# Performance work log

Measured on AMD Instinct MI355X. Metric: run time of the kernel, lower is better.

## Reference

```python
import jax, jax.numpy as jnp
import numpy as np
import math

B, S, D, H = 4, 2048, 1024, 16
DK = D // H
DFF = 1024  # FeedForward default d_ff=1024 (DecoderLayer passes only d_model)
EPS = 1e-6
SQRT_2_OVER_PI = math.sqrt(2.0 / math.pi)


def setup_inputs() -> dict:
    key = jax.random.key(0)
    ks = jax.random.split(key, 12)
    sc = 0.02
    x = jax.random.normal(ks[0], (B, S, D), dtype=jnp.float32)
    # causal look-ahead mask: 1 where attendable, 0 where masked
    mask = jnp.broadcast_to(jnp.tril(jnp.ones((S, S), dtype=jnp.int32)), (B, S, S))
    inp = {
        'x': x,
        'mask': mask,
        'Wq': jax.random.normal(ks[1], (D, D), jnp.float32) * sc,
        'bq': jnp.zeros((D,), jnp.float32),
        'Wk': jax.random.normal(ks[2], (D, D), jnp.float32) * sc,
        'bk': jnp.zeros((D,), jnp.float32),
        'Wv': jax.random.normal(ks[3], (D, D), jnp.float32) * sc,
        'bv': jnp.zeros((D,), jnp.float32),
        'Wo': jax.random.normal(ks[4], (D, D), jnp.float32) * sc,
        'bo': jnp.zeros((D,), jnp.float32),
        'W1': jax.random.normal(ks[5], (D, DFF), jnp.float32) * sc,
        'b1': jnp.zeros((DFF,), jnp.float32),
        'W2': jax.random.normal(ks[6], (DFF, D), jnp.float32) * sc,
        'b2': jnp.zeros((D,), jnp.float32),
        'alpha1': jnp.ones((D,), jnp.float32),
        'bias1': jnp.zeros((D,), jnp.float32),
        'alpha2': jnp.ones((D,), jnp.float32),
        'bias2': jnp.zeros((D,), jnp.float32),
    }
    return inp


def _norm(x, alpha, bias):
    # torch: (x - mean) / (x.std(unbiased=True) + eps) * alpha + bias
    mean = jnp.mean(x, axis=-1, keepdims=True)
    var = jnp.sum((x - mean) ** 2, axis=-1, keepdims=True) / (x.shape[-1] - 1)
    std = jnp.sqrt(var)
    return alpha * (x - mean) / (std + EPS) + bias


def _gelu(x):
    return 0.5 * x * (1.0 + jnp.tanh(SQRT_2_OVER_PI * (x + 0.044715 * x ** 3)))


def reference(x, mask, Wq, bq, Wk, bk, Wv, bv, Wo, bo, W1, b1, W2, b2,
              alpha1, bias1, alpha2, bias2):
    b, s, d = x.shape
    x2 = _norm(x, alpha1, bias1)
    q = (x2 @ Wq + bq).reshape(b, s, H, DK).transpose(0, 2, 1, 3)  # bhsd
    k = (x2 @ Wk + bk).reshape(b, s, H, DK).transpose(0, 2, 1, 3)
    v = (x2 @ Wv + bv).reshape(b, s, H, DK).transpose(0, 2, 1, 3)
    scores = jnp.einsum('bhqd,bhkd->bhqk', q, k) / jnp.sqrt(jnp.float32(DK))
    scores = jnp.where(mask[:, None, :, :] == 0, jnp.float32(-1e9), scores)
    probs = jax.nn.softmax(scores, axis=-1)
    attn = jnp.einsum('bhqk,bhkd->bhqd', probs, v)
    concat = attn.transpose(0, 2, 1, 3).reshape(b, s, d)
    x = x + (concat @ Wo + bo)
    x2 = _norm(x, alpha2, bias2)
    ff = _gelu(x2 @ W1 + b1) @ W2 + b2
    return x + ff
```

## Files before the change

### kernel.cpp

```cpp
#include <hip/hip_runtime.h>
#include <hip/hip_bf16.h>
#include <math.h>


#define B_ 4
#define S_ 2048
#define D_ 1024
#define H_ 16
#define DFF_ 1024

typedef __attribute__((ext_vector_type(8))) short short8;
typedef __attribute__((ext_vector_type(8))) unsigned short ushort8;
typedef __attribute__((ext_vector_type(4))) float f32x4;

__device__ __forceinline__ unsigned short f2bf(float f) {
  __hip_bfloat16 h = __float2bfloat16(f);
  return *reinterpret_cast<unsigned short*>(&h);
}

__device__ __forceinline__ void gload16(const void* g, void* l) {
  __builtin_amdgcn_global_load_lds(
      (const __attribute__((address_space(1))) void*)g,
      (__attribute__((address_space(3))) void*)l, 16, 0, 0);
}

__global__ __launch_bounds__(256) void tcast6_k(
    const float* s0, const float* s1, const float* s2, const float* s3,
    const float* s4, const float* s5, unsigned short* d0, unsigned short* d1,
    unsigned short* d2, unsigned short* d3, unsigned short* d4,
    unsigned short* d5) {
  const float* src;
  unsigned short* dst;
  switch (blockIdx.z) {
    case 0: src = s0; dst = d0; break;
    case 1: src = s1; dst = d1; break;
    case 2: src = s2; dst = d2; break;
    case 3: src = s3; dst = d3; break;
    case 4: src = s4; dst = d4; break;
    default: src = s5; dst = d5; break;
  }
  __shared__ float tile[64][65];
  const int k0 = blockIdx.y * 64, n0 = blockIdx.x * 64;
  const int t = threadIdx.x;
  const int r = t >> 2, c0 = (t & 3) * 16;
  const float4* sp =
      reinterpret_cast<const float4*>(src + (size_t)(k0 + r) * 1024 + n0 + c0);
#pragma unroll
  for (int j = 0; j < 4; ++j) {
    float4 v = sp[j];
    tile[r][c0 + 4 * j] = v.x;
    tile[r][c0 + 4 * j + 1] = v.y;
    tile[r][c0 + 4 * j + 2] = v.z;
    tile[r][c0 + 4 * j + 3] = v.w;
  }
  __syncthreads();
  ushort8 o0, o1;
#pragma unroll
  for (int j = 0; j < 8; ++j) o0[j] = f2bf(tile[c0 + j][r]);
#pragma unroll
  for (int j = 0; j < 8; ++j) o1[j] = f2bf(tile[c0 + 8 + j][r]);
  unsigned short* dp = dst + (size_t)(n0 + r) * 1024 + k0 + c0;
  *reinterpret_cast<ushort8*>(dp) = o0;
  *reinterpret_cast<ushort8*>(dp + 8) = o1;
}

__global__ __launch_bounds__(256) void ln_k(const float* __restrict__ x,
                                            const float* __restrict__ alpha,
                                            const float* __restrict__ bias,
                                            unsigned short* __restrict__ out) {
  int row = blockIdx.x, t = threadIdx.x;
  float4 v = reinterpret_cast<const float4*>(x + (size_t)row * D_)[t];
  float s = v.x + v.y + v.z + v.w;
  float q = v.x * v.x + v.y * v.y + v.z * v.z + v.w * v.w;
#pragma unroll
  for (int off = 32; off > 0; off >>= 1) {
    s += __shfl_down(s, off);
    q += __shfl_down(q, off);
  }
  __shared__ float ss[4], sq[4], stat[2];
  if ((t & 63) == 0) { ss[t >> 6] = s; sq[t >> 6] = q; }
  __syncthreads();
  if (t == 0) {
    float S = ss[0] + ss[1] + ss[2] + ss[3];
    float Q = sq[0] + sq[1] + sq[2] + sq[3];
    float mean = S * (1.0f / D_);
    float var = fmaxf((Q - D_ * mean * mean) * (1.0f / (D_ - 1)), 0.0f);
    stat[0] = mean;
    stat[1] = 1.0f / (sqrtf(var) + 1e-6f);
  }
  __syncthreads();
  float mean = stat[0], inv = stat[1];
  float4 a = reinterpret_cast<const float4*>(alpha)[t];
  float4 b = reinterpret_cast<const float4*>(bias)[t];
  ushort4 o;
  o.x = f2bf((v.x - mean) * inv * a.x + b.x);
  o.y = f2bf((v.y - mean) * inv * a.y + b.y);
  o.z = f2bf((v.z - mean) * inv * a.z + b.z);
  o.w = f2bf((v.w - mean) * inv * a.w + b.w);
  reinterpret_cast<ushort4*>(out + (size_t)row * D_)[t] = o;
}

__device__ __forceinline__ void gemm_core64(
    const unsigned short* __restrict__ A, const unsigned short* __restrict__ Wt,
    int m0, int n0, int K, unsigned short* As ,
    unsigned short* Bs , f32x4 (&acc)[2][4]) {
  const int t = threadIdx.x;
  const int wv = t >> 6, lane = t & 63, quad = lane >> 4, l16 = lane & 15;
  const int wm = wv >> 1, wn = wv & 1;
  const int lr8 = lane >> 3;
  const int lseg = ((lane & 7) ^ lr8) * 8;

  const unsigned short* Ag0 = A + (size_t)(m0 + wv * 16 + lr8) * K + lseg;
  const unsigned short* Ag1 = A + (size_t)(m0 + wv * 16 + 8 + lr8) * K + lseg;
  const unsigned short* Bg0 = Wt + (size_t)(n0 + wv * 32 + lr8) * K + lseg;
  const unsigned short* Bg1 = Wt + (size_t)(n0 + wv * 32 + 8 + lr8) * K + lseg;
  const unsigned short* Bg2 = Wt + (size_t)(n0 + wv * 32 + 16 + lr8) * K + lseg;
  const unsigned short* Bg3 = Wt + (size_t)(n0 + wv * 32 + 24 + lr8) * K + lseg;
  unsigned short* Al0 = &As[(wv * 16) * 64];
  unsigned short* Al1 = &As[(wv * 16 + 8) * 64];
  unsigned short* Bl0 = &Bs[(wv * 32) * 64];
  unsigned short* Bl1 = &Bs[(wv * 32 + 8) * 64];
  unsigned short* Bl2 = &Bs[(wv * 32 + 16) * 64];
  unsigned short* Bl3 = &Bs[(wv * 32 + 24) * 64];

  for (int k0 = 0; k0 < K; k0 += 64) {
    gload16(Ag0, Al0);
    gload16(Ag1, Al1);
    gload16(Bg0, Bl0);
    gload16(Bg1, Bl1);
    gload16(Bg2, Bl2);
    gload16(Bg3, Bl3);
    __syncthreads();
    short8 af[2][2], bf[2][4];
#pragma unroll
    for (int p = 0; p < 2; ++p) {
#pragma unroll
      for (int mt = 0; mt < 2; ++mt) {
        int r = wm * 32 + mt * 16 + l16;
        af[p][mt] = *reinterpret_cast<const short8*>(
            &As[r * 64 + (((p * 4 + quad) ^ (r & 7)) << 3)]);
      }
#pragma unroll
      for (int nt = 0; nt < 4; ++nt) {
        int r = wn * 64 + nt * 16 + l16;
        bf[p][nt] = *reinterpret_cast<const short8*>(
            &Bs[r * 64 + (((p * 4 + quad) ^ (r & 7)) << 3)]);
      }
    }
#pragma unroll
    for (int p = 0; p < 2; ++p)
#pragma unroll
      for (int mt = 0; mt < 2; ++mt)
#pragma unroll
        for (int nt = 0; nt < 4; ++nt)
          acc[mt][nt] = __builtin_amdgcn_mfma_f32_16x16x32_bf16(
              af[p][mt], bf[p][nt], acc[mt][nt], 0, 0, 0);
    __syncthreads();
    Ag0 += 64; Ag1 += 64; Bg0 += 64; Bg1 += 64; Bg2 += 64; Bg3 += 64;
  }
}

__global__ __launch_bounds__(256, 4) void gemm_k(
    const unsigned short* __restrict__ A, const unsigned short* __restrict__ Wt,
    const float* __restrict__ bias, const float* __restrict__ res,
    void* __restrict__ outp, int M, int N, int K, int flags) {
  __shared__ unsigned short As[64 * 64];
  __shared__ unsigned short Bs[128 * 64];
  const int t = threadIdx.x;
  const int m0 = blockIdx.y * 64, n0 = blockIdx.x * 128;
  const int wv = t >> 6, lane = t & 63, quad = lane >> 4, l16 = lane & 15;
  const int wm = wv >> 1, wn = wv & 1;
  f32x4 acc[2][4] = {};
  gemm_core64(A, Wt, m0, n0, K, As, Bs, acc);

  const bool obf = flags & 1, dog = flags & 2;
#pragma unroll
  for (int nt = 0; nt < 4; ++nt) {
    int col = n0 + wn * 64 + nt * 16 + l16;
    float bv = bias[col];
#pragma unroll
    for (int mt = 0; mt < 2; ++mt) {
#pragma unroll
      for (int r = 0; r < 4; ++r) {
        int row = m0 + wm * 32 + mt * 16 + quad * 4 + r;
        float v = acc[mt][nt][r] + bv;
        if (res) v += res[(size_t)row * N + col];
        if (dog) {
          float e = __expf(1.5957691216057308f * (v + 0.044715f * v * v * v));
          float th = 1.0f - 2.0f / (1.0f + e);
          v = 0.5f * v * (1.0f + th);
        }
        if (obf)
          ((unsigned short*)outp)[(size_t)row * N + col] = f2bf(v);
        else
          ((float*)outp)[(size_t)row * N + col] = v;
      }
    }
  }
}

__global__ __launch_bounds__(256, 4) void gemmqkv_k(
    const unsigned short* __restrict__ A, const unsigned short* __restrict__ Wt,
    const float* __restrict__ bq, const float* __restrict__ bk,
    const float* __restrict__ bv, unsigned short* __restrict__ outq,
    unsigned short* __restrict__ outk, unsigned short* __restrict__ outvt,
    int M, int K) {
  __shared__ unsigned short As[64 * 64];
  __shared__ unsigned short Bs[128 * 64];
  const int t = threadIdx.x;
  const int m0 = blockIdx.y * 64, n0 = blockIdx.x * 128;
  const int wv = t >> 6, lane = t & 63, quad = lane >> 4, l16 = lane & 15;
  const int wm = wv >> 1, wn = wv & 1;
  f32x4 acc[2][4] = {};
  gemm_core64(A, Wt, m0, n0, K, As, Bs, acc);

  const int seg = n0 >> 10;
  const int nb = n0 & 1023;
  const float* bias = (seg == 0) ? bq : (seg == 1) ? bk : bv;
  if (seg < 2) {
    unsigned short* o = (seg == 0) ? outq : outk;
#pragma unroll
    for (int nt = 0; nt < 4; ++nt) {
      int col = nb + wn * 64 + nt * 16 + l16;
      float bvv = bias[col];
#pragma unroll
      for (int mt = 0; mt < 2; ++mt)
#pragma unroll
        for (int r = 0; r < 4; ++r) {
          int row = m0 + wm * 32 + mt * 16 + quad * 4 + r;
          o[(size_t)row * D_ + col] = f2bf(acc[mt][nt][r] + bvv);
        }
    }
  } else {
#pragma unroll
    for (int nt = 0; nt < 4; ++nt) {
      int col = nb + wn * 64 + nt * 16 + l16;
      float bvv = bias[col];
      int h = col >> 6, dk = col & 63;
#pragma unroll
      for (int mt = 0; mt < 2; ++mt) {
        int m = m0 + wm * 32 + mt * 16 + quad * 4;
        int b = m >> 11, sidx = m & 2047;
        ushort4 o;
        o.x = f2bf(acc[mt][nt][0] + bvv);
        o.y = f2bf(acc[mt][nt][1] + bvv);
        o.z = f2bf(acc[mt][nt][2] + bvv);
        o.w = f2bf(acc[mt][nt][3] + bvv);
        *reinterpret_cast<ushort4*>(
            &outvt[(((size_t)(b * 16 + h) * 64 + dk) * 2048 + sidx)]) = o;
      }
    }
  }
}

__global__ __launch_bounds__(256, 2) void attn_k(
    const unsigned short* __restrict__ Q, const unsigned short* __restrict__ Kg,
    const unsigned short* __restrict__ VT, unsigned short* __restrict__ Og) {
  __shared__ unsigned short Ks[2][64 * 64];
  __shared__ unsigned short Vs[2][64 * 64];
  __shared__ unsigned short Ps[4 * 32 * 72];
  const int t = threadIdx.x;
  const int pair = blockIdx.x >> 6, bh = blockIdx.x & 63;
  const int b = bh >> 4, h = bh & 15;
  const int hi = 31 - pair, lo = pair;
  const int w = t >> 6, lane = t & 63, quad = lane >> 4, l16 = lane & 15;
  const int qhi0 = hi * 64 + w * 16, qlo0 = lo * 64 + w * 16;
  unsigned short* PsW = &Ps[w * 32 * 72];

  short8 qfh[2], qfl[2];
#pragma unroll
  for (int kc = 0; kc < 2; ++kc) {
    qfh[kc] = *reinterpret_cast<const short8*>(
        Q + (size_t)(b * S_ + qhi0 + l16) * D_ + h * 64 + kc * 32 + quad * 8);
    qfl[kc] = *reinterpret_cast<const short8*>(
        Q + (size_t)(b * S_ + qlo0 + l16) * D_ + h * 64 + kc * 32 + quad * 8);
  }
  asm volatile("" ::"v"(qfh[0]), "v"(qfh[1]), "v"(qfl[0]), "v"(qfl[1])
               : "memory");

  f32x4 Oh[4] = {}, Ol[4] = {};
  float lh_acc = 0.0f, ll_acc = 0.0f;

  const int srA = w * 8 + (lane >> 3);
  const int ssA = ((lane & 7) ^ (srA & 7)) * 8;
  const int srB = srA + 32;
  const int ssB = ((lane & 7) ^ (srB & 7)) * 8;
  const unsigned short* KgA = Kg + (size_t)(b * S_ + srA) * D_ + h * 64 + ssA;
  const unsigned short* KgB = Kg + (size_t)(b * S_ + srB) * D_ + h * 64 + ssB;
  const unsigned short* VgA = VT + ((size_t)bh * 64 + srA) * 2048 + ssA;
  const unsigned short* VgB = VT + ((size_t)bh * 64 + srB) * 2048 + ssB;
  unsigned short* KlA = &Ks[0][(w * 8) * 64];
  unsigned short* KlB = &Ks[0][(32 + w * 8) * 64];
  unsigned short* VlA = &Vs[0][(w * 8) * 64];
  unsigned short* VlB = &Vs[0][(32 + w * 8) * 64];

  const float C0 = 0.18033688011f;
  const float C1 = -23.08312065f;

  gload16(KgA, KlA);
  gload16(KgB, KlB);
  gload16(VgA, VlA);
  gload16(VgB, VlB);
  KgA += (size_t)64 * D_;
  KgB += (size_t)64 * D_;
  VgA += 64;
  VgB += 64;

  for (int kt = 0; kt <= hi; ++kt) {
    const int k0 = kt * 64;
    const bool dolo = (kt <= lo);
    const int coff = (kt & 1) << 12;
    const int noff = ((kt & 1) ^ 1) << 12;

    if (kt < hi) {
      gload16(KgA, KlA + noff);
      gload16(KgB, KlB + noff);
      gload16(VgA, VlA + noff);
      gload16(VgB, VlB + noff);
      KgA += (size_t)64 * D_;
      KgB += (size_t)64 * D_;
      VgA += 64;
      VgB += 64;
      asm volatile("s_waitcnt vmcnt(4)" ::: "memory");
    } else {
      asm volatile("s_waitcnt vmcnt(0)" ::: "memory");
    }
    asm volatile("s_barrier" ::: "memory");

    const unsigned short* Ksc = &Ks[0][coff];
    const unsigned short* Vsc = &Vs[0][coff];

    f32x4 sch[4] = {}, scl[4] = {};
#pragma unroll
    for (int mt = 0; mt < 4; ++mt) {
      int r = mt * 16 + l16;
      short8 kf0 = *reinterpret_cast<const short8*>(
          &Ksc[r * 64 + ((quad ^ (r & 7)) << 3)]);
      short8 kf1 = *reinterpret_cast<const short8*>(
          &Ksc[r * 64 + (((4 + quad) ^ (r & 7)) << 3)]);
      sch[mt] = __builtin_amdgcn_mfma_f32_16x16x32_bf16(kf0, qfh[0], sch[mt],
                                                        0, 0, 0);
      sch[mt] = __builtin_amdgcn_mfma_f32_16x16x32_bf16(kf1, qfh[1], sch[mt],
                                                        0, 0, 0);
      if (dolo) {
        scl[mt] = __builtin_amdgcn_mfma_f32_16x16x32_bf16(kf0, qfl[0], scl[mt],
                                                          0, 0, 0);
        scl[mt] = __builtin_amdgcn_mfma_f32_16x16x32_bf16(kf1, qfl[1], scl[mt],
                                                          0, 0, 0);
      }
    }

    {
      const bool diag = (kt == hi);
      const int q = qhi0 + l16;
#pragma unroll
      for (int mt = 0; mt < 4; ++mt) {
        float pv[4];
#pragma unroll
        for (int r = 0; r < 4; ++r) {
          int key = k0 + mt * 16 + quad * 4 + r;
          float p = __builtin_amdgcn_exp2f(fmaf(sch[mt][r], C0, C1));
          if (diag && key > q) p = 0.0f;
          lh_acc += p;
          pv[r] = p;
        }
        ushort4 pk = {f2bf(pv[0]), f2bf(pv[1]), f2bf(pv[2]), f2bf(pv[3])};
        *reinterpret_cast<ushort4*>(&PsW[l16 * 72 + mt * 16 + quad * 4]) = pk;
      }
    }
    if (dolo) {
      const bool diag = (kt == lo);
      const int q = qlo0 + l16;
#pragma unroll
      for (int mt = 0; mt < 4; ++mt) {
        float pv[4];
#pragma unroll
        for (int r = 0; r < 4; ++r) {
          int key = k0 + mt * 16 + quad * 4 + r;
          float p = __builtin_amdgcn_exp2f(fmaf(scl[mt][r], C0, C1));
          if (diag && key > q) p = 0.0f;
          ll_acc += p;
          pv[r] = p;
        }
        ushort4 pk = {f2bf(pv[0]), f2bf(pv[1]), f2bf(pv[2]), f2bf(pv[3])};
        *reinterpret_cast<ushort4*>(
            &PsW[(16 + l16) * 72 + mt * 16 + quad * 4]) = pk;
      }
    }
    __builtin_amdgcn_sched_barrier(0);

    short8 pfh[2], pfl[2];
#pragma unroll
    for (int kc = 0; kc < 2; ++kc)
      pfh[kc] = *reinterpret_cast<const short8*>(
          &PsW[l16 * 72 + kc * 32 + quad * 8]);
    if (dolo) {
#pragma unroll
      for (int kc = 0; kc < 2; ++kc)
        pfl[kc] = *reinterpret_cast<const short8*>(
            &PsW[(16 + l16) * 72 + kc * 32 + quad * 8]);
    }

#pragma unroll
    for (int kc = 0; kc < 2; ++kc) {
#pragma unroll
      for (int nd = 0; nd < 4; ++nd) {
        int r = nd * 16 + l16;
        short8 vf = *reinterpret_cast<const short8*>(
            &Vsc[r * 64 + (((kc * 4 + quad) ^ (r & 7)) << 3)]);
        Oh[nd] = __builtin_amdgcn_mfma_f32_16x16x32_bf16(pfh[kc], vf, Oh[nd],
                                                         0, 0, 0);
        if (dolo)
          Ol[nd] = __builtin_amdgcn_mfma_f32_16x16x32_bf16(pfl[kc], vf, Ol[nd],
                                                           0, 0, 0);
      }
    }
    asm volatile("s_barrier" ::: "memory");
  }

  lh_acc += __shfl_xor(lh_acc, 16);
  lh_acc += __shfl_xor(lh_acc, 32);
  ll_acc += __shfl_xor(ll_acc, 16);
  ll_acc += __shfl_xor(ll_acc, 32);

#pragma unroll
  for (int r = 0; r < 4; ++r) {
    float lh = __shfl(lh_acc, quad * 4 + r);
    float ll = __shfl(ll_acc, quad * 4 + r);
    float rlh = 1.0f / lh, rll = 1.0f / ll;
#pragma unroll
    for (int nd = 0; nd < 4; ++nd) {
      Og[(size_t)(b * S_ + qhi0 + quad * 4 + r) * D_ + h * 64 + nd * 16 + l16] =
          f2bf(Oh[nd][r] * rlh);
      Og[(size_t)(b * S_ + qlo0 + quad * 4 + r) * D_ + h * 64 + nd * 16 + l16] =
          f2bf(Ol[nd][r] * rll);
    }
  }
}

extern "C" void kernel_launch(void* const* d_in, const int* in_sizes, int n_in,
                              void* d_out, int out_size, void* d_ws,
                              size_t ws_size, hipStream_t stream) {
  const float* x = (const float*)d_in[0];
  const float* Wq = (const float*)d_in[2];
  const float* bq = (const float*)d_in[3];
  const float* Wk = (const float*)d_in[4];
  const float* bk = (const float*)d_in[5];
  const float* Wv = (const float*)d_in[6];
  const float* bv = (const float*)d_in[7];
  const float* Wo = (const float*)d_in[8];
  const float* bo = (const float*)d_in[9];
  const float* W1 = (const float*)d_in[10];
  const float* b1 = (const float*)d_in[11];
  const float* W2 = (const float*)d_in[12];
  const float* b2 = (const float*)d_in[13];
  const float* alpha1 = (const float*)d_in[14];
  const float* bias1 = (const float*)d_in[15];
  const float* alpha2 = (const float*)d_in[16];
  const float* bias2 = (const float*)d_in[17];
  float* out = (float*)d_out;

  char* ws = (char*)d_ws;
  const size_t MB = 1024 * 1024;
  unsigned short* wqT = (unsigned short*)(ws + 0 * MB);
  unsigned short* wkT = (unsigned short*)(ws + 2 * MB);
  unsigned short* wvT = (unsigned short*)(ws + 4 * MB);
  unsigned short* woT = (unsigned short*)(ws + 6 * MB);
  unsigned short* w1T = (unsigned short*)(ws + 8 * MB);
  unsigned short* w2T = (unsigned short*)(ws + 10 * MB);
  unsigned short* x2a = (unsigned short*)(ws + 12 * MB);
  unsigned short* qb = (unsigned short*)(ws + 28 * MB);
  unsigned short* kb = (unsigned short*)(ws + 44 * MB);
  unsigned short* vtb = (unsigned short*)(ws + 60 * MB);

  tcast6_k<<<dim3(16, 16, 6), dim3(256), 0, stream>>>(Wq, Wk, Wv, Wo, W1, W2,
                                                      wqT, wkT, wvT, woT, w1T,
                                                      w2T);

  const int M = B_ * S_;
  ln_k<<<dim3(M), dim3(256), 0, stream>>>(x, alpha1, bias1, x2a);

  gemmqkv_k<<<dim3(24, 128), dim3(256), 0, stream>>>(x2a, wqT, bq, bk, bv, qb,
                                                     kb, vtb, M, D_);

  attn_k<<<dim3(1024), dim3(256), 0, stream>>>(qb, kb, vtb, x2a);

  dim3 gg(D_ / 128, M / 64);
  gemm_k<<<gg, dim3(256), 0, stream>>>(x2a, woT, bo, x, out, M, D_, D_, 0);

  ln_k<<<dim3(M), dim3(256), 0, stream>>>(out, alpha2, bias2, qb);

  gemm_k<<<gg, dim3(256), 0, stream>>>(qb, w1T, b1, nullptr, kb, M, DFF_, D_, 3);

  gemm_k<<<gg, dim3(256), 0, stream>>>(kb, w2T, b2, out, out, M, D_, DFF_, 0);
}
```

Measured before the change: 429.8 us.

## Split paired hi/lo attention blocks into one query tile per block; MFMA row sums

The attention kernel no longer pairs a high and a low query tile in one block. It launches 2048 blocks, each handling a single 64-query tile, ordered longest-first. The softmax denominator is now computed with an extra MFMA against a vector of ones, replacing the scalar accumulation and cross-lane shuffles. This raises parallelism and cuts register and LDS use, but each K/V tile loaded from memory now serves fewer queries and the causal work per block is uneven. The denominator also now sums bf16-rounded probabilities.

```diff
diff --git a/kernel.cpp b/kernel.cpp
--- a/kernel.cpp
+++ b/kernel.cpp
@@ -258,28 +258,27 @@
     const unsigned short* __restrict__ VT, unsigned short* __restrict__ Og) {
   __shared__ unsigned short Ks[2][64 * 64];
   __shared__ unsigned short Vs[2][64 * 64];
-  __shared__ unsigned short Ps[4 * 32 * 72];
+  __shared__ unsigned short Ps[4 * 16 * 72];
   const int t = threadIdx.x;
-  const int pair = blockIdx.x >> 6, bh = blockIdx.x & 63;
+  const int qt = 31 - (blockIdx.x >> 6);
+  const int bh = blockIdx.x & 63;
   const int b = bh >> 4, h = bh & 15;
-  const int hi = 31 - pair, lo = pair;
   const int w = t >> 6, lane = t & 63, quad = lane >> 4, l16 = lane & 15;
-  const int qhi0 = hi * 64 + w * 16, qlo0 = lo * 64 + w * 16;
-  unsigned short* PsW = &Ps[w * 32 * 72];
-
-  short8 qfh[2], qfl[2];
-#pragma unroll
-  for (int kc = 0; kc < 2; ++kc) {
-    qfh[kc] = *reinterpret_cast<const short8*>(
-        Q + (size_t)(b * S_ + qhi0 + l16) * D_ + h * 64 + kc * 32 + quad * 8);
-    qfl[kc] = *reinterpret_cast<const short8*>(
-        Q + (size_t)(b * S_ + qlo0 + l16) * D_ + h * 64 + kc * 32 + quad * 8);
-  }
-  asm volatile("" ::"v"(qfh[0]), "v"(qfh[1]), "v"(qfl[0]), "v"(qfl[1])
-               : "memory");
-
-  f32x4 Oh[4] = {}, Ol[4] = {};
-  float lh_acc = 0.0f, ll_acc = 0.0f;
+  const int q0 = qt * 64 + w * 16;
+  unsigned short* PsW = &Ps[w * 16 * 72];
+
+  short8 qf[2];
+#pragma unroll
+  for (int kc = 0; kc < 2; ++kc)
+    qf[kc] = *reinterpret_cast<const short8*>(
+        Q + (size_t)(b * S_ + q0 + l16) * D_ + h * 64 + kc * 32 + quad * 8);
+  asm volatile("" ::"v"(qf[0]), "v"(qf[1]) : "memory");
+
+  f32x4 Oh[4] = {};
+  f32x4 sums = {};
+  short8 onev;
+#pragma unroll
+  for (int j = 0; j < 8; ++j) onev[j] = (short)0x3F80;
 
   const int srA = w * 8 + (lane >> 3);
   const int ssA = ((lane & 7) ^ (srA & 7)) * 8;
@@ -306,13 +305,12 @@
   VgA += 64;
   VgB += 64;
 
-  for (int kt = 0; kt <= hi; ++kt) {
-    const int k0 = kt * 64;
-    const bool dolo = (kt <= lo);
+  for (int kt = 0; kt <= qt; ++kt) {
+    const bool diag = (kt == qt);
     const int coff = (kt & 1) << 12;
     const int noff = ((kt & 1) ^ 1) << 12;
 
-    if (kt < hi) {
+    if (kt < qt) {
       gload16(KgA, KlA + noff);
       gload16(KgB, KlB + noff);
       gload16(VgA, VlA + noff);
@@ -330,7 +328,7 @@
     const unsigned short* Ksc = &Ks[0][coff];
     const unsigned short* Vsc = &Vs[0][coff];
 
-    f32x4 sch[4] = {}, scl[4] = {};
+    f32x4 sch[4] = {};
 #pragma unroll
     for (int mt = 0; mt < 4; ++mt) {
       int r = mt * 16 + l16;
@@ -338,103 +336,60 @@
           &Ksc[r * 64 + ((quad ^ (r & 7)) << 3)]);
       short8 kf1 = *reinterpret_cast<const short8*>(
           &Ksc[r * 64 + (((4 + quad) ^ (r & 7)) << 3)]);
-      sch[mt] = __builtin_amdgcn_mfma_f32_16x16x32_bf16(kf0, qfh[0], sch[mt],
+      sch[mt] = __builtin_amdgcn_mfma_f32_16x16x32_bf16(kf0, qf[0], sch[mt],
                                                         0, 0, 0);
-      sch[mt] = __builtin_amdgcn_mfma_f32_16x16x32_bf16(kf1, qfh[1], sch[mt],
+      sch[mt] = __builtin_amdgcn_mfma_f32_16x16x32_bf16(kf1, qf[1], sch[mt],
                                                         0, 0, 0);
-      if (dolo) {
-        scl[mt] = __builtin_amdgcn_mfma_f32_16x16x32_bf16(kf0, qfl[0], scl[mt],
-                                                          0, 0, 0);
-        scl[mt] = __builtin_amdgcn_mfma_f32_16x16x32_bf16(kf1, qfl[1], scl[mt],
-                                                          0, 0, 0);
-      }
     }
 
     {
-      const bool diag = (kt == hi);
-      const int q = qhi0 + l16;
+      const int kb0 = kt * 64;
+      const int q = q0 + l16;
 #pragma unroll
       for (int mt = 0; mt < 4; ++mt) {
         float pv[4];
 #pragma unroll
         for (int r = 0; r < 4; ++r) {
-          int key = k0 + mt * 16 + quad * 4 + r;
+          int key = kb0 + mt * 16 + quad * 4 + r;
           float p = __builtin_amdgcn_exp2f(fmaf(sch[mt][r], C0, C1));
           if (diag && key > q) p = 0.0f;
-          lh_acc += p;
           pv[r] = p;
         }
         ushort4 pk = {f2bf(pv[0]), f2bf(pv[1]), f2bf(pv[2]), f2bf(pv[3])};
         *reinterpret_cast<ushort4*>(&PsW[l16 * 72 + mt * 16 + quad * 4]) = pk;
       }
     }
-    if (dolo) {
-      const bool diag = (kt == lo);
-      const int q = qlo0 + l16;
-#pragma unroll
-      for (int mt = 0; mt < 4; ++mt) {
-        float pv[4];
-#pragma unroll
-        for (int r = 0; r < 4; ++r) {
-          int key = k0 + mt * 16 + quad * 4 + r;
-          float p = __builtin_amdgcn_exp2f(fmaf(scl[mt][r], C0, C1));
-          if (diag && key > q) p = 0.0f;
-          ll_acc += p;
-          pv[r] = p;
-        }
-        ushort4 pk = {f2bf(pv[0]), f2bf(pv[1]), f2bf(pv[2]), f2bf(pv[3])};
-        *reinterpret_cast<ushort4*>(
-            &PsW[(16 + l16) * 72 + mt * 16 + quad * 4]) = pk;
-      }
-    }
     __builtin_amdgcn_sched_barrier(0);
 
-    short8 pfh[2], pfl[2];
+    short8 pf[2];
 #pragma unroll
     for (int kc = 0; kc < 2; ++kc)
-      pfh[kc] = *reinterpret_cast<const short8*>(
+      pf[kc] = *reinterpret_cast<const short8*>(
           &PsW[l16 * 72 + kc * 32 + quad * 8]);
-    if (dolo) {
-#pragma unroll
-      for (int kc = 0; kc < 2; ++kc)
-        pfl[kc] = *reinterpret_cast<const short8*>(
-            &PsW[(16 + l16) * 72 + kc * 32 + quad * 8]);
-    }
 
 #pragma unroll
     for (int kc = 0; kc < 2; ++kc) {
+      sums = __builtin_amdgcn_mfma_f32_16x16x32_bf16(pf[kc], onev, sums,
+                                                     0, 0, 0);
 #pragma unroll
       for (int nd = 0; nd < 4; ++nd) {
         int r = nd * 16 + l16;
         short8 vf = *reinterpret_cast<const short8*>(
             &Vsc[r * 64 + (((kc * 4 + quad) ^ (r & 7)) << 3)]);
-        Oh[nd] = __builtin_amdgcn_mfma_f32_16x16x32_bf16(pfh[kc], vf, Oh[nd],
+        Oh[nd] = __builtin_amdgcn_mfma_f32_16x16x32_bf16(pf[kc], vf, Oh[nd],
                                                          0, 0, 0);
-        if (dolo)
-          Ol[nd] = __builtin_amdgcn_mfma_f32_16x16x32_bf16(pfl[kc], vf, Ol[nd],
-                                                           0, 0, 0);
       }
     }
     asm volatile("s_barrier" ::: "memory");
   }
 
-  lh_acc += __shfl_xor(lh_acc, 16);
-  lh_acc += __shfl_xor(lh_acc, 32);
-  ll_acc += __shfl_xor(ll_acc, 16);
-  ll_acc += __shfl_xor(ll_acc, 32);
-
 #pragma unroll
   for (int r = 0; r < 4; ++r) {
-    float lh = __shfl(lh_acc, quad * 4 + r);
-    float ll = __shfl(ll_acc, quad * 4 + r);
-    float rlh = 1.0f / lh, rll = 1.0f / ll;
-#pragma unroll
-    for (int nd = 0; nd < 4; ++nd) {
-      Og[(size_t)(b * S_ + qhi0 + quad * 4 + r) * D_ + h * 64 + nd * 16 + l16] =
-          f2bf(Oh[nd][r] * rlh);
-      Og[(size_t)(b * S_ + qlo0 + quad * 4 + r) * D_ + h * 64 + nd * 16 + l16] =
-          f2bf(Ol[nd][r] * rll);
-    }
+    float rl = 1.0f / sums[r];
+#pragma unroll
+    for (int nd = 0; nd < 4; ++nd)
+      Og[(size_t)(b * S_ + q0 + quad * 4 + r) * D_ + h * 64 + nd * 16 + l16] =
+          f2bf(Oh[nd][r] * rl);
   }
 }
 
@@ -483,7 +438,7 @@
   gemmqkv_k<<<dim3(24, 128), dim3(256), 0, stream>>>(x2a, wqT, bq, bk, bv, qb,
                                                      kb, vtb, M, D_);
 
-  attn_k<<<dim3(1024), dim3(256), 0, stream>>>(qb, kb, vtb, x2a);
+  attn_k<<<dim3(2048), dim3(256), 0, stream>>>(qb, kb, vtb, x2a);
 
   dim3 gg(D_ / 128, M / 64);
   gemm_k<<<gg, dim3(256), 0, stream>>>(x2a, woT, bo, x, out, M, D_, D_, 0);
```

After: 403.1 us. 1.07x faster.
